# Kernel optimization log

Hardware: AMD Instinct MI355X
Metric: run time of the kernel (lower is better)

## Reference

```python
import jax, jax.numpy as jnp
import numpy as np

N, E, F, D, C, L, H = 50000, 800000, 256, 128, 40, 5, 8
HD = D // H
EPS = 1e-5


def setup_inputs() -> dict:
    key = jax.random.key(0)
    keys = iter(jax.random.split(key, 40))
    def w(shape, fan_in):
        return jax.random.normal(next(keys), shape, jnp.float32) / np.sqrt(fan_in)
    return dict(
        x=jax.random.normal(next(keys), (N, F), jnp.float32),
        edge_src=jax.random.randint(next(keys), (E,), 0, N, jnp.int32),
        edge_dst=jax.random.randint(next(keys), (E,), 0, N, jnp.int32),
        Wi=w((F, D), F), bi=jnp.zeros((D,), jnp.float32),
        Wq=w((L, D, D), D), bq=jnp.zeros((L, D), jnp.float32),
        Wk=w((L, D, D), D), bk=jnp.zeros((L, D), jnp.float32),
        Wv=w((L, D, D), D), bv=jnp.zeros((L, D), jnp.float32),
        Wo=w((L, D, D), D), bo=jnp.zeros((L, D), jnp.float32),
        g1=jnp.ones((L, D), jnp.float32), b1=jnp.zeros((L, D), jnp.float32),
        Wf1=w((L, D, 2 * D), D), bf1=jnp.zeros((L, 2 * D), jnp.float32),
        Wf2=w((L, 2 * D, D), 2 * D), bf2=jnp.zeros((L, D), jnp.float32),
        g_out=jnp.ones((D,), jnp.float32), b_out=jnp.zeros((D,), jnp.float32),
        Wout=w((D, C), D), bout=jnp.zeros((C,), jnp.float32),
    )


def _ln(x, g, b):
    mu = x.mean(-1, keepdims=True)
    var = ((x - mu) ** 2).mean(-1, keepdims=True)
    return (x - mu) / jnp.sqrt(var + EPS) * g + b


def _attn(h, src, dst, Wq, bq, Wk, bk, Wv, bv, Wo, bo):
    n = h.shape[0]
    q = (h @ Wq + bq).reshape(n, H, HD)
    k = (h @ Wk + bk).reshape(n, H, HD)
    v = (h @ Wv + bv).reshape(n, H, HD)
    # u_dot_v: per-edge dot(q[src], k[dst]) per head -> [E, H]
    scores = jnp.einsum('ehd,ehd->eh', q[src], k[dst]) / np.sqrt(HD).astype(np.float32)
    # edge_softmax over incoming edges of each destination node
    m = jax.ops.segment_max(scores, dst, num_segments=n)
    ex = jnp.exp(scores - m[dst])
    denom = jax.ops.segment_sum(ex, dst, num_segments=n)
    p = ex / denom[dst]
    # u_mul_e_sum: sum_e v[src] * p  scattered to dst
    agg = jax.ops.segment_sum(v[src] * p[:, :, None], dst, num_segments=n)
    return agg.reshape(n, D) @ Wo + bo


def reference(x, edge_src, edge_dst, Wi, bi, Wq, bq, Wk, bk, Wv, bv, Wo, bo,
              g1, b1, Wf1, bf1, Wf2, bf2, g_out, b_out, Wout, bout):
    h = jax.nn.relu(x @ Wi + bi)
    for i in range(L):
        r = _ln(h, g1[i], b1[i])
        r = _attn(r, edge_src, edge_dst, Wq[i], bq[i], Wk[i], bk[i], Wv[i], bv[i], Wo[i], bo[i])
        h = h + r
        # NOTE: original module reuses norms_1 here (norms_2 unused) - reproduced
        r = _ln(h, g1[i], b1[i])
        r = jax.nn.relu(r @ Wf1[i] + bf1[i]) @ Wf2[i] + bf2[i]
        h = h + r
    mid = h
    out = _ln(h, g_out, b_out) @ Wout + bout  # squeeze(1) is a no-op (nclass != 1)
    return (mid, out)
```

## Files before the change

kernel.cpp:

```cpp
#include <hip/hip_runtime.h>
#include <hip/hip_bf16.h>

typedef __hip_bfloat16 bf16;
typedef __attribute__((ext_vector_type(8))) short bf16x8;
typedef __attribute__((ext_vector_type(4))) float f32x4;

#define N_NODES 50000
#define N_EDGES 800000
#define DIM 128
#define QKVW 384

__device__ __forceinline__ void storeO(float* p, float v){ *p = v; }
__device__ __forceinline__ void storeO(bf16* p, float v){ *p = __float2bfloat16(v); }
__device__ __forceinline__ float bfu2f(unsigned short u){
  return __uint_as_float(((unsigned)u) << 16);
}
__device__ __forceinline__ unsigned short f2bfbits(float f){
  bf16 t = __float2bfloat16(f);
  return *reinterpret_cast<unsigned short*>(&t);
}

__global__ void fill_kernel(unsigned* __restrict__ p, unsigned val, int n){
  int i = blockIdx.x * blockDim.x + threadIdx.x;
  if (i < n) p[i] = val;
}

__global__ void prep_w_kernel(const float* __restrict__ W, bf16* __restrict__ Wt,
    int K, int M, int L){
  int idx = blockIdx.x * blockDim.x + threadIdx.x;
  int tot = L * K * M;
  if (idx >= tot) return;
  int l = idx / (K * M), r = idx - l * (K * M);
  int m = r / K, k = r - m * K;
  Wt[idx] = __float2bfloat16(W[(size_t)l * K * M + (size_t)k * M + m]);
}

__global__ void prep_qkvw_kernel(const float* __restrict__ Wq, const float* __restrict__ Wk,
    const float* __restrict__ Wv, bf16* __restrict__ Wt){
  int idx = blockIdx.x * blockDim.x + threadIdx.x;
  if (idx >= 5 * QKVW * 128) return;
  int l = idx / (QKVW * 128), r = idx - l * (QKVW * 128);
  int m = r / 128, k = r - m * 128;
  const float* src = (m < 128) ? (Wq + (size_t)l * 16384 + (size_t)k * 128 + m)
                   : (m < 256) ? (Wv + (size_t)l * 16384 + (size_t)k * 128 + (m - 128))
                               : (Wk + (size_t)l * 16384 + (size_t)k * 128 + (m - 256));
  Wt[idx] = __float2bfloat16(*src);
}

__global__ void pack_qkvbias_kernel(const float* __restrict__ bq, const float* __restrict__ bk,
    const float* __restrict__ bv, float* __restrict__ bqkv){
  int i = blockIdx.x * blockDim.x + threadIdx.x;
  if (i >= 5 * QKVW) return;
  int l = i / QKVW, j = i - l * QKVW;
  float v = (j < 128) ? bq[l * 128 + j] : (j < 256) ? bv[l * 128 + j - 128] : bk[l * 128 + j - 256];
  bqkv[i] = v;
}

__global__ void hist_kernel(const int* __restrict__ dst, int* __restrict__ counts, int E){
  int e = blockIdx.x * blockDim.x + threadIdx.x;
  if (e < E) atomicAdd(counts + dst[e], 1);
}

__global__ __launch_bounds__(256) void blockscan_kernel(const int* __restrict__ counts,
    int* __restrict__ rowptr, int* __restrict__ bsum, int n){
  __shared__ int buf[256];
  int t = threadIdx.x, i = blockIdx.x * 256 + t;
  int x = (i < n) ? counts[i] : 0;
  buf[t] = x; __syncthreads();
  #pragma unroll
  for (int off = 1; off < 256; off <<= 1){
    int v = (t >= off) ? buf[t - off] : 0;
    __syncthreads(); buf[t] += v; __syncthreads();
  }
  if (i < n) rowptr[i] = buf[t] - x;
  if (t == 255) bsum[blockIdx.x] = buf[255];
}

__global__ __launch_bounds__(256) void scanb_kernel(int* __restrict__ bsum, int nb){
  __shared__ int buf[256];
  int t = threadIdx.x;
  int x = (t < nb) ? bsum[t] : 0;
  buf[t] = x; __syncthreads();
  #pragma unroll
  for (int off = 1; off < 256; off <<= 1){
    int v = (t >= off) ? buf[t - off] : 0;
    __syncthreads(); buf[t] += v; __syncthreads();
  }
  if (t < nb) bsum[t] = buf[t] - x;
  if (t == nb - 1) bsum[nb] = buf[t];
}

__global__ void addoff_kernel(int* __restrict__ rowptr, const int* __restrict__ bsum,
    int n, int nb){
  int i = blockIdx.x * blockDim.x + threadIdx.x;
  if (i < n) rowptr[i] += bsum[i >> 8];
  if (i == 0) rowptr[n] = bsum[nb];
}

__global__ void scatter_kernel(const int* __restrict__ src, const int* __restrict__ dst,
    const int* __restrict__ rowptr, int* __restrict__ cursor,
    int* __restrict__ srclist, int E){
  int e = blockIdx.x * blockDim.x + threadIdx.x;
  if (e >= E) return;
  int d = dst[e];
  int pos = rowptr[d] + atomicAdd(cursor + d, 1);
  srclist[pos] = src[e];
}

__global__ __launch_bounds__(256) void attn_kernel(
    const int* __restrict__ rowptr, const int* __restrict__ srclist,
    const bf16* __restrict__ qkv, bf16* __restrict__ agg, int n){
  int d = blockIdx.x * 4 + (threadIdx.x >> 6);
  int lane = threadIdx.x & 63;
  if (d >= n) return;
  int eslot = lane >> 4;
  int t = lane & 15;
  float kf[8];
  {
    const int4* kp = (const int4*)(qkv + (size_t)d * QKVW + 256 + t * 8);
    int4 kv = kp[0];
    const unsigned* ku = (const unsigned*)&kv;
    #pragma unroll
    for (int j = 0; j < 4; j++){
      kf[2*j]   = __uint_as_float(ku[j] << 16) * 0.25f;
      kf[2*j+1] = __uint_as_float(ku[j] & 0xffff0000u) * 0.25f;
    }
  }
  float acc[8];
  #pragma unroll
  for (int j = 0; j < 8; j++) acc[j] = 0.f;
  float den = 0.f;
  int e = rowptr[d], e1 = rowptr[d + 1];
  for (; e < e1; e += 8){
    int eeA = e + eslot, eeB = e + 4 + eslot;
    int sA = srclist[(eeA < e1) ? eeA : (e1 - 1)];
    int sB = srclist[(eeB < e1) ? eeB : (e1 - 1)];
    const int4* qpA = (const int4*)(qkv + (size_t)sA * QKVW + t * 8);
    const int4* qpB = (const int4*)(qkv + (size_t)sB * QKVW + t * 8);
    int4 qA = qpA[0];
    int4 vA = qpA[16];
    int4 qB = qpB[0];
    int4 vB = qpB[16];
    float pA = 0.f, pB = 0.f;
    const unsigned* qa = (const unsigned*)&qA;
    const unsigned* qb = (const unsigned*)&qB;
    #pragma unroll
    for (int j = 0; j < 4; j++){
      pA = fmaf(__uint_as_float(qa[j] << 16),          kf[2*j],   pA);
      pA = fmaf(__uint_as_float(qa[j] & 0xffff0000u),  kf[2*j+1], pA);
      pB = fmaf(__uint_as_float(qb[j] << 16),          kf[2*j],   pB);
      pB = fmaf(__uint_as_float(qb[j] & 0xffff0000u),  kf[2*j+1], pB);
    }
    pA += __shfl_xor(pA, 1);
    pB += __shfl_xor(pB, 1);
    float wA = (eeA < e1) ? __expf(pA) : 0.f;
    float wB = (eeB < e1) ? __expf(pB) : 0.f;
    den += wA + wB;
    const unsigned* va = (const unsigned*)&vA;
    const unsigned* vb = (const unsigned*)&vB;
    #pragma unroll
    for (int j = 0; j < 4; j++){
      acc[2*j]   = fmaf(wA, __uint_as_float(va[j] << 16),         acc[2*j]);
      acc[2*j+1] = fmaf(wA, __uint_as_float(va[j] & 0xffff0000u), acc[2*j+1]);
      acc[2*j]   = fmaf(wB, __uint_as_float(vb[j] << 16),         acc[2*j]);
      acc[2*j+1] = fmaf(wB, __uint_as_float(vb[j] & 0xffff0000u), acc[2*j+1]);
    }
  }
  #pragma unroll
  for (int m = 16; m <= 32; m <<= 1){
    den += __shfl_xor(den, m);
    #pragma unroll
    for (int j = 0; j < 8; j++) acc[j] += __shfl_xor(acc[j], m);
  }
  if (eslot == 0){
    float inv = (den > 0.f) ? 1.f / den : 0.f;
    unsigned short o[8];
    #pragma unroll
    for (int j = 0; j < 8; j++) o[j] = f2bfbits(acc[j] * inv);
    *(int4*)(agg + (size_t)d * DIM + t * 8) = *(const int4*)o;
  }
}

template<int KT, int MT, typename AT, bool FUSELN, bool RELU, bool RESID, typename OT>
__global__ __launch_bounds__(256, (KT == 128) ? 4 : 2) void pgemm4(
    const AT* __restrict__ A, const float* __restrict__ lng, const float* __restrict__ lnb,
    const bf16* __restrict__ Wt, const float* __restrict__ bias,
    const float* __restrict__ resid, OT* __restrict__ out, float* __restrict__ out2,
    int n, int M){
  constexpr int CPR = KT / 8;
  constexpr int CPT = (64 * CPR) / 256;
  constexpr int NMT = MT / 64;
  constexpr int NKS = KT / 32;
  __shared__ short Ash[64][KT + 8];
  int tid = threadIdx.x;
  int wv = tid >> 6, lane = tid & 63;
  int l15 = lane & 15, quad = lane >> 4;
  int bm = blockIdx.x * 64;

  bf16x8 wf[2][NKS];
  auto loadW = [&](int mt, int b){
    int col = mt * 64 + wv * 16 + l15;
    #pragma unroll
    for (int ks = 0; ks < NKS; ks++){
      int4 w = make_int4(0, 0, 0, 0);
      if (col < M) w = *(const int4*)(Wt + (size_t)col * KT + ks * 32 + quad * 8);
      wf[b][ks] = *(bf16x8*)&w;
    }
  };
  loadW(0, 0);

  #pragma unroll
  for (int i = 0; i < CPT; i++){
    int c = tid + i * 256;
    int row = c / CPR, off = (c - row * CPR) * 8;
    int gr = bm + row;
    if constexpr (sizeof(AT) == 4){
      float va[8];
      if (gr < n){
        float4 f0 = *(const float4*)(A + (size_t)gr * KT + off);
        float4 f1 = *(const float4*)(A + (size_t)gr * KT + off + 4);
        va[0]=f0.x; va[1]=f0.y; va[2]=f0.z; va[3]=f0.w;
        va[4]=f1.x; va[5]=f1.y; va[6]=f1.z; va[7]=f1.w;
      } else {
        #pragma unroll
        for (int j = 0; j < 8; j++) va[j] = 0.f;
      }
      if constexpr (FUSELN){
        float s = va[0]+va[1]+va[2]+va[3]+va[4]+va[5]+va[6]+va[7];
        s += __shfl_xor(s, 1); s += __shfl_xor(s, 2);
        s += __shfl_xor(s, 4); s += __shfl_xor(s, 8);
        float mu = s * (1.f / 128.f);
        float vs = 0.f;
        #pragma unroll
        for (int j = 0; j < 8; j++){ float dd = va[j] - mu; vs += dd * dd; }
        vs += __shfl_xor(vs, 1); vs += __shfl_xor(vs, 2);
        vs += __shfl_xor(vs, 4); vs += __shfl_xor(vs, 8);
        float rs = rsqrtf(vs * (1.f / 128.f) + 1e-5f);
        float4 g0 = *(const float4*)(lng + off);
        float4 g1 = *(const float4*)(lng + off + 4);
        float4 b0 = *(const float4*)(lnb + off);
        float4 b1 = *(const float4*)(lnb + off + 4);
        va[0]=(va[0]-mu)*rs*g0.x+b0.x; va[1]=(va[1]-mu)*rs*g0.y+b0.y;
        va[2]=(va[2]-mu)*rs*g0.z+b0.z; va[3]=(va[3]-mu)*rs*g0.w+b0.w;
        va[4]=(va[4]-mu)*rs*g1.x+b1.x; va[5]=(va[5]-mu)*rs*g1.y+b1.y;
        va[6]=(va[6]-mu)*rs*g1.z+b1.z; va[7]=(va[7]-mu)*rs*g1.w+b1.w;
      }
      unsigned short tmp[8];
      #pragma unroll
      for (int j = 0; j < 8; j++) tmp[j] = f2bfbits(va[j]);
      *(int4*)(&Ash[row][off]) = *(const int4*)tmp;
    } else {
      int4 av = make_int4(0, 0, 0, 0);
      if (gr < n) av = *(const int4*)(A + (size_t)gr * KT + off);
      *(int4*)(&Ash[row][off]) = av;
    }
  }
  __syncthreads();

  #pragma unroll
  for (int mt = 0; mt < NMT; mt++){
    int b = mt & 1;
    if (mt + 1 < NMT) loadW(mt + 1, b ^ 1);
    f32x4 acc[4];
    #pragma unroll
    for (int i = 0; i < 4; i++) acc[i] = (f32x4){0.f, 0.f, 0.f, 0.f};
    #pragma unroll
    for (int ks = 0; ks < NKS; ks++){
      bf16x8 bfrag = wf[b][ks];
      #pragma unroll
      for (int mi = 0; mi < 4; mi++){
        bf16x8 afrag = *(const bf16x8*)(&Ash[mi * 16 + l15][ks * 32 + quad * 8]);
        acc[mi] = __builtin_amdgcn_mfma_f32_16x16x32_bf16(afrag, bfrag, acc[mi], 0, 0, 0);
      }
    }
    int col = mt * 64 + wv * 16 + l15;
    if (col < M){
      float bval = bias[col];
      #pragma unroll
      for (int mi = 0; mi < 4; mi++){
        int row0 = bm + mi * 16 + quad * 4;
        #pragma unroll
        for (int rg = 0; rg < 4; rg++){
          int grow = row0 + rg;
          if (grow >= n) continue;
          float v = acc[mi][rg] + bval;
          if (RELU) v = fmaxf(v, 0.f);
          if (RESID) v += resid[(size_t)grow * M + col];
          storeO(out + (size_t)grow * M + col, v);
          if (out2) out2[(size_t)grow * M + col] = v;
        }
      }
    }
  }
}

extern "C" void kernel_launch(void* const* d_in, const int* in_sizes, int n_in,
                              void* d_out, int out_size, void* d_ws, size_t ws_size,
                              hipStream_t stream) {
  const float* x    = (const float*)d_in[0];
  const int*  esrc  = (const int*)d_in[1];
  const int*  edst  = (const int*)d_in[2];
  const float* Wi   = (const float*)d_in[3];
  const float* bi   = (const float*)d_in[4];
  const float* Wq   = (const float*)d_in[5];
  const float* bq   = (const float*)d_in[6];
  const float* Wk   = (const float*)d_in[7];
  const float* bk   = (const float*)d_in[8];
  const float* Wv   = (const float*)d_in[9];
  const float* bv   = (const float*)d_in[10];
  const float* Wo   = (const float*)d_in[11];
  const float* bo   = (const float*)d_in[12];
  const float* g1   = (const float*)d_in[13];
  const float* b1   = (const float*)d_in[14];
  const float* Wf1  = (const float*)d_in[15];
  const float* bf1  = (const float*)d_in[16];
  const float* Wf2  = (const float*)d_in[17];
  const float* bf2  = (const float*)d_in[18];
  const float* gout = (const float*)d_in[19];
  const float* bout_ln = (const float*)d_in[20];
  const float* Wout = (const float*)d_in[21];
  const float* bout = (const float*)d_in[22];

  const size_t ND = (size_t)N_NODES * DIM;
  float* ws = (float*)d_ws;
  float* h   = ws;
  bf16* agg  = (bf16*)(ws + ND);
  bf16* qkv  = (bf16*)(ws + ND + ND / 2);
  bf16* mid  = qkv;
  float* after_qkv = ws + ND + ND / 2 + ((size_t)N_NODES * QKVW) / 2;
  bf16* Wit    = (bf16*)after_qkv;
  bf16* Wqkvt  = Wit + 128 * 256;
  bf16* Wot    = Wqkvt + 5 * QKVW * 128;
  bf16* Wf1t   = Wot + 5 * 128 * 128;
  bf16* Wf2t   = Wf1t + 5 * 256 * 128;
  bf16* Woutt  = Wf2t + 5 * 128 * 256;
  float* bqkv  = (float*)(Woutt + 40 * 128);
  int* rowptr  = (int*)(bqkv + 5 * QKVW);
  int* cnt     = rowptr + N_NODES + 1;
  int* bsum    = cnt + N_NODES;
  int* srclist = bsum + 200;

  dim3 B(256);
  const int EB = (N_EDGES + 255) / 256;
  const int NB = (N_NODES + 255) / 256;
  const int NSB = (N_NODES + 255) / 256;
  dim3 Grow(782);

  prep_w_kernel<<<(1 * 256 * 128 + 255) / 256, B, 0, stream>>>(Wi, Wit, 256, 128, 1);
  prep_qkvw_kernel<<<(5 * QKVW * 128 + 255) / 256, B, 0, stream>>>(Wq, Wk, Wv, Wqkvt);
  prep_w_kernel<<<(5 * 128 * 128 + 255) / 256, B, 0, stream>>>(Wo, Wot, 128, 128, 5);
  prep_w_kernel<<<(5 * 128 * 256 + 255) / 256, B, 0, stream>>>(Wf1, Wf1t, 128, 256, 5);
  prep_w_kernel<<<(5 * 256 * 128 + 255) / 256, B, 0, stream>>>(Wf2, Wf2t, 256, 128, 5);
  prep_w_kernel<<<(1 * 128 * 40 + 255) / 256, B, 0, stream>>>(Wout, Woutt, 128, 40, 1);
  pack_qkvbias_kernel<<<(5 * QKVW + 255) / 256, B, 0, stream>>>(bq, bk, bv, bqkv);
  fill_kernel<<<NB, B, 0, stream>>>((unsigned*)cnt, 0u, N_NODES);
  hist_kernel<<<EB, B, 0, stream>>>(edst, cnt, N_EDGES);
  blockscan_kernel<<<NSB, B, 0, stream>>>(cnt, rowptr, bsum, N_NODES);
  scanb_kernel<<<1, B, 0, stream>>>(bsum, NSB);
  addoff_kernel<<<NB, B, 0, stream>>>(rowptr, bsum, N_NODES, NSB);
  fill_kernel<<<NB, B, 0, stream>>>((unsigned*)cnt, 0u, N_NODES);
  scatter_kernel<<<EB, B, 0, stream>>>(esrc, edst, rowptr, cnt, srclist, N_EDGES);

  pgemm4<256, 128, float, false, true, false, float><<<Grow, B, 0, stream>>>(
      x, nullptr, nullptr, Wit, bi, nullptr, h, nullptr, N_NODES, 128);

  for (int l = 0; l < 5; l++){
    pgemm4<128, 384, float, true, false, false, bf16><<<Grow, B, 0, stream>>>(
        h, g1 + l * DIM, b1 + l * DIM, Wqkvt + (size_t)l * QKVW * 128,
        bqkv + l * QKVW, nullptr, qkv, nullptr, N_NODES, QKVW);
    attn_kernel<<<12500, B, 0, stream>>>(rowptr, srclist, qkv, agg, N_NODES);
    pgemm4<128, 128, bf16, false, false, true, float><<<Grow, B, 0, stream>>>(
        agg, nullptr, nullptr, Wot + (size_t)l * 128 * 128, bo + l * DIM,
        h, h, nullptr, N_NODES, 128);
    pgemm4<128, 256, float, true, true, false, bf16><<<Grow, B, 0, stream>>>(
        h, g1 + l * DIM, b1 + l * DIM, Wf1t + (size_t)l * 256 * 128,
        bf1 + l * 2 * DIM, nullptr, mid, nullptr, N_NODES, 256);
    float* out2 = (l == 4) ? (float*)d_out : nullptr;
    pgemm4<256, 128, bf16, false, false, true, float><<<Grow, B, 0, stream>>>(
        mid, nullptr, nullptr, Wf2t + (size_t)l * 128 * 256, bf2 + l * DIM,
        h, h, out2, N_NODES, 128);
  }

  pgemm4<128, 64, float, true, false, false, float><<<Grow, B, 0, stream>>>(
      h, gout, bout_ln, Woutt, bout, nullptr, ((float*)d_out) + ND, nullptr, N_NODES, 40);
}
```

Baseline: 1.060 ms.

## Fuse consecutive GEMMs through shared-memory LayerNorm into a two-stage kernel

Replaces the single-GEMM kernel with a fused kernel that computes a 128-wide GEMM with bias, residual and ReLU, writes h, then LayerNorms the tile in shared memory and runs the following GEMM (QKV, FFN1 or output head). This chains input-proj→QKV, Wo→FFN1 and FFN2→next QKV or head, so h is never re-read from global memory for the LN-fused GEMMs, and the launch count drops. It uses more shared memory and registers per block and computes variance as E[x²]−mu², which is less numerically stable. The mid buffer is moved to its own region so it no longer aliases qkv.

```diff
diff --git a/kernel.cpp b/kernel.cpp
--- a/kernel.cpp
+++ b/kernel.cpp
@@ -181,113 +181,183 @@
   }
 }
 
-template<int KT, int MT, typename AT, bool FUSELN, bool RELU, bool RESID, typename OT>
-__global__ __launch_bounds__(256, (KT == 128) ? 4 : 2) void pgemm4(
-    const AT* __restrict__ A, const float* __restrict__ lng, const float* __restrict__ lnb,
-    const bf16* __restrict__ Wt, const float* __restrict__ bias,
-    const float* __restrict__ resid, OT* __restrict__ out, float* __restrict__ out2,
-    int n, int M){
-  constexpr int CPR = KT / 8;
+template<int KT1, typename AT1, bool RELU1, bool RESID, int M2T, bool RELU2, typename OT2>
+__global__ __launch_bounds__(256, (KT1 == 128) ? 4 : 3) void fgemm(
+    const AT1* __restrict__ A, const bf16* __restrict__ W1t, const float* __restrict__ b1v,
+    const float* __restrict__ resid, float* __restrict__ hout, float* __restrict__ outd,
+    const float* __restrict__ lng, const float* __restrict__ lnb,
+    const bf16* __restrict__ W2t, const float* __restrict__ b2v,
+    OT2* __restrict__ out2nd, int n, int M2rt){
+  constexpr int NKS1 = KT1 / 32;
+  constexpr int NMT2 = M2T / 64;
+  constexpr int CPR = KT1 / 8;
   constexpr int CPT = (64 * CPR) / 256;
-  constexpr int NMT = MT / 64;
-  constexpr int NKS = KT / 32;
-  __shared__ short Ash[64][KT + 8];
+  __shared__ short Ash[64][KT1 + 8];
+  __shared__ short Ash2[64][136];
+  __shared__ float2 sred[4][64];
   int tid = threadIdx.x;
   int wv = tid >> 6, lane = tid & 63;
   int l15 = lane & 15, quad = lane >> 4;
   int bm = blockIdx.x * 64;
 
-  bf16x8 wf[2][NKS];
-  auto loadW = [&](int mt, int b){
+  bf16x8 wf[NKS1];
+  auto loadW1 = [&](int mt){
     int col = mt * 64 + wv * 16 + l15;
     #pragma unroll
-    for (int ks = 0; ks < NKS; ks++){
-      int4 w = make_int4(0, 0, 0, 0);
-      if (col < M) w = *(const int4*)(Wt + (size_t)col * KT + ks * 32 + quad * 8);
-      wf[b][ks] = *(bf16x8*)&w;
+    for (int ks = 0; ks < NKS1; ks++){
+      int4 w = *(const int4*)(W1t + (size_t)col * KT1 + ks * 32 + quad * 8);
+      wf[ks] = *(bf16x8*)&w;
     }
   };
-  loadW(0, 0);
+  loadW1(0);
 
   #pragma unroll
   for (int i = 0; i < CPT; i++){
     int c = tid + i * 256;
     int row = c / CPR, off = (c - row * CPR) * 8;
     int gr = bm + row;
-    if constexpr (sizeof(AT) == 4){
+    if constexpr (sizeof(AT1) == 4){
       float va[8];
       if (gr < n){
-        float4 f0 = *(const float4*)(A + (size_t)gr * KT + off);
-        float4 f1 = *(const float4*)(A + (size_t)gr * KT + off + 4);
+        float4 f0 = *(const float4*)(A + (size_t)gr * KT1 + off);
+        float4 f1 = *(const float4*)(A + (size_t)gr * KT1 + off + 4);
         va[0]=f0.x; va[1]=f0.y; va[2]=f0.z; va[3]=f0.w;
         va[4]=f1.x; va[5]=f1.y; va[6]=f1.z; va[7]=f1.w;
       } else {
         #pragma unroll
         for (int j = 0; j < 8; j++) va[j] = 0.f;
       }
-      if constexpr (FUSELN){
-        float s = va[0]+va[1]+va[2]+va[3]+va[4]+va[5]+va[6]+va[7];
-        s += __shfl_xor(s, 1); s += __shfl_xor(s, 2);
-        s += __shfl_xor(s, 4); s += __shfl_xor(s, 8);
-        float mu = s * (1.f / 128.f);
-        float vs = 0.f;
-        #pragma unroll
-        for (int j = 0; j < 8; j++){ float dd = va[j] - mu; vs += dd * dd; }
-        vs += __shfl_xor(vs, 1); vs += __shfl_xor(vs, 2);
-        vs += __shfl_xor(vs, 4); vs += __shfl_xor(vs, 8);
-        float rs = rsqrtf(vs * (1.f / 128.f) + 1e-5f);
-        float4 g0 = *(const float4*)(lng + off);
-        float4 g1 = *(const float4*)(lng + off + 4);
-        float4 b0 = *(const float4*)(lnb + off);
-        float4 b1 = *(const float4*)(lnb + off + 4);
-        va[0]=(va[0]-mu)*rs*g0.x+b0.x; va[1]=(va[1]-mu)*rs*g0.y+b0.y;
-        va[2]=(va[2]-mu)*rs*g0.z+b0.z; va[3]=(va[3]-mu)*rs*g0.w+b0.w;
-        va[4]=(va[4]-mu)*rs*g1.x+b1.x; va[5]=(va[5]-mu)*rs*g1.y+b1.y;
-        va[6]=(va[6]-mu)*rs*g1.z+b1.z; va[7]=(va[7]-mu)*rs*g1.w+b1.w;
-      }
       unsigned short tmp[8];
       #pragma unroll
       for (int j = 0; j < 8; j++) tmp[j] = f2bfbits(va[j]);
       *(int4*)(&Ash[row][off]) = *(const int4*)tmp;
     } else {
       int4 av = make_int4(0, 0, 0, 0);
-      if (gr < n) av = *(const int4*)(A + (size_t)gr * KT + off);
+      if (gr < n) av = *(const int4*)(A + (size_t)gr * KT1 + off);
       *(int4*)(&Ash[row][off]) = av;
     }
   }
   __syncthreads();
 
-  #pragma unroll
-  for (int mt = 0; mt < NMT; mt++){
-    int b = mt & 1;
-    if (mt + 1 < NMT) loadW(mt + 1, b ^ 1);
-    f32x4 acc[4];
-    #pragma unroll
-    for (int i = 0; i < 4; i++) acc[i] = (f32x4){0.f, 0.f, 0.f, 0.f};
-    #pragma unroll
-    for (int ks = 0; ks < NKS; ks++){
-      bf16x8 bfrag = wf[b][ks];
+  f32x4 acc[2][4];
+  #pragma unroll
+  for (int mt = 0; mt < 2; mt++)
+    #pragma unroll
+    for (int mi = 0; mi < 4; mi++) acc[mt][mi] = (f32x4){0.f, 0.f, 0.f, 0.f};
+  #pragma unroll
+  for (int mt = 0; mt < 2; mt++){
+    if (mt) loadW1(1);
+    #pragma unroll
+    for (int ks = 0; ks < NKS1; ks++){
+      bf16x8 bfrag = wf[ks];
       #pragma unroll
       for (int mi = 0; mi < 4; mi++){
         bf16x8 afrag = *(const bf16x8*)(&Ash[mi * 16 + l15][ks * 32 + quad * 8]);
-        acc[mi] = __builtin_amdgcn_mfma_f32_16x16x32_bf16(afrag, bfrag, acc[mi], 0, 0, 0);
-      }
-    }
+        acc[mt][mi] = __builtin_amdgcn_mfma_f32_16x16x32_bf16(afrag, bfrag, acc[mt][mi], 0, 0, 0);
+      }
+    }
+  }
+
+  int colv[2] = { wv * 16 + l15, 64 + wv * 16 + l15 };
+  float b1c[2] = { b1v[colv[0]], b1v[colv[1]] };
+  #pragma unroll
+  for (int mt = 0; mt < 2; mt++){
+    #pragma unroll
+    for (int mi = 0; mi < 4; mi++){
+      #pragma unroll
+      for (int rg = 0; rg < 4; rg++){
+        int grow = bm + mi * 16 + quad * 4 + rg;
+        float v = acc[mt][mi][rg] + b1c[mt];
+        if (RESID && grow < n) v += resid[(size_t)grow * 128 + colv[mt]];
+        if (RELU1) v = fmaxf(v, 0.f);
+        acc[mt][mi][rg] = v;
+        if (grow < n){
+          hout[(size_t)grow * 128 + colv[mt]] = v;
+          if (outd) outd[(size_t)grow * 128 + colv[mt]] = v;
+        }
+      }
+    }
+  }
+  #pragma unroll
+  for (int mi = 0; mi < 4; mi++){
+    #pragma unroll
+    for (int rg = 0; rg < 4; rg++){
+      float s = acc[0][mi][rg] + acc[1][mi][rg];
+      float q = acc[0][mi][rg] * acc[0][mi][rg] + acc[1][mi][rg] * acc[1][mi][rg];
+      s += __shfl_xor(s, 1); q += __shfl_xor(q, 1);
+      s += __shfl_xor(s, 2); q += __shfl_xor(q, 2);
+      s += __shfl_xor(s, 4); q += __shfl_xor(q, 4);
+      s += __shfl_xor(s, 8); q += __shfl_xor(q, 8);
+      if (l15 == 0) sred[wv][mi * 16 + quad * 4 + rg] = make_float2(s, q);
+    }
+  }
+  __syncthreads();
+  if (tid < 64){
+    float2 a0 = sred[0][tid], a1 = sred[1][tid], a2 = sred[2][tid], a3 = sred[3][tid];
+    float s = a0.x + a1.x + a2.x + a3.x;
+    float q = a0.y + a1.y + a2.y + a3.y;
+    float mu = s * (1.f / 128.f);
+    float var = q * (1.f / 128.f) - mu * mu;
+    float rs = rsqrtf(fmaxf(var, 0.f) + 1e-5f);
+    sred[0][tid] = make_float2(mu, rs);
+  }
+  __syncthreads();
+  float gg[2] = { lng[colv[0]], lng[colv[1]] };
+  float bb[2] = { lnb[colv[0]], lnb[colv[1]] };
+  #pragma unroll
+  for (int mi = 0; mi < 4; mi++){
+    #pragma unroll
+    for (int rg = 0; rg < 4; rg++){
+      int row = mi * 16 + quad * 4 + rg;
+      float2 ms = sred[0][row];
+      #pragma unroll
+      for (int mt = 0; mt < 2; mt++){
+        float hv = (acc[mt][mi][rg] - ms.x) * ms.y * gg[mt] + bb[mt];
+        Ash2[row][colv[mt]] = (short)f2bfbits(hv);
+      }
+    }
+  }
+  __syncthreads();
+
+  bf16x8 wf2[2][4];
+  auto loadW2 = [&](int mt, int b){
     int col = mt * 64 + wv * 16 + l15;
-    if (col < M){
-      float bval = bias[col];
+    #pragma unroll
+    for (int ks = 0; ks < 4; ks++){
+      int4 w = make_int4(0, 0, 0, 0);
+      if (col < M2rt) w = *(const int4*)(W2t + (size_t)col * 128 + ks * 32 + quad * 8);
+      wf2[b][ks] = *(bf16x8*)&w;
+    }
+  };
+  loadW2(0, 0);
+  #pragma unroll
+  for (int mt = 0; mt < NMT2; mt++){
+    int b = mt & 1;
+    if (mt + 1 < NMT2) loadW2(mt + 1, b ^ 1);
+    f32x4 a2[4];
+    #pragma unroll
+    for (int i = 0; i < 4; i++) a2[i] = (f32x4){0.f, 0.f, 0.f, 0.f};
+    #pragma unroll
+    for (int ks = 0; ks < 4; ks++){
+      bf16x8 bfrag = wf2[b][ks];
       #pragma unroll
       for (int mi = 0; mi < 4; mi++){
-        int row0 = bm + mi * 16 + quad * 4;
+        bf16x8 afrag = *(const bf16x8*)(&Ash2[mi * 16 + l15][ks * 32 + quad * 8]);
+        a2[mi] = __builtin_amdgcn_mfma_f32_16x16x32_bf16(afrag, bfrag, a2[mi], 0, 0, 0);
+      }
+    }
+    int col = mt * 64 + wv * 16 + l15;
+    if (col < M2rt){
+      float bval = b2v[col];
+      #pragma unroll
+      for (int mi = 0; mi < 4; mi++){
         #pragma unroll
         for (int rg = 0; rg < 4; rg++){
-          int grow = row0 + rg;
+          int grow = bm + mi * 16 + quad * 4 + rg;
           if (grow >= n) continue;
-          float v = acc[mi][rg] + bval;
-          if (RELU) v = fmaxf(v, 0.f);
-          if (RESID) v += resid[(size_t)grow * M + col];
-          storeO(out + (size_t)grow * M + col, v);
-          if (out2) out2[(size_t)grow * M + col] = v;
+          float v = a2[mi][rg] + bval;
+          if (RELU2) v = fmaxf(v, 0.f);
+          storeO(out2nd + (size_t)grow * M2rt + col, v);
         }
       }
     }
@@ -326,9 +396,9 @@
   float* h   = ws;
   bf16* agg  = (bf16*)(ws + ND);
   bf16* qkv  = (bf16*)(ws + ND + ND / 2);
-  bf16* mid  = qkv;
-  float* after_qkv = ws + ND + ND / 2 + ((size_t)N_NODES * QKVW) / 2;
-  bf16* Wit    = (bf16*)after_qkv;
+  bf16* mid  = qkv + (size_t)N_NODES * QKVW;
+  float* after_mid = ws + ND + ND / 2 + ((size_t)N_NODES * (QKVW + 256)) / 2;
+  bf16* Wit    = (bf16*)after_mid;
   bf16* Wqkvt  = Wit + 128 * 256;
   bf16* Wot    = Wqkvt + 5 * QKVW * 128;
   bf16* Wf1t   = Wot + 5 * 128 * 128;
@@ -361,26 +431,27 @@
   fill_kernel<<<NB, B, 0, stream>>>((unsigned*)cnt, 0u, N_NODES);
   scatter_kernel<<<EB, B, 0, stream>>>(esrc, edst, rowptr, cnt, srclist, N_EDGES);
 
-  pgemm4<256, 128, float, false, true, false, float><<<Grow, B, 0, stream>>>(
-      x, nullptr, nullptr, Wit, bi, nullptr, h, nullptr, N_NODES, 128);
+  fgemm<256, float, true, false, 384, false, bf16><<<Grow, B, 0, stream>>>(
+      x, Wit, bi, nullptr, h, nullptr, g1, b1,
+      Wqkvt, bqkv, qkv, N_NODES, QKVW);
 
   for (int l = 0; l < 5; l++){
-    pgemm4<128, 384, float, true, false, false, bf16><<<Grow, B, 0, stream>>>(
-        h, g1 + l * DIM, b1 + l * DIM, Wqkvt + (size_t)l * QKVW * 128,
-        bqkv + l * QKVW, nullptr, qkv, nullptr, N_NODES, QKVW);
     attn_kernel<<<12500, B, 0, stream>>>(rowptr, srclist, qkv, agg, N_NODES);
-    pgemm4<128, 128, bf16, false, false, true, float><<<Grow, B, 0, stream>>>(
-        agg, nullptr, nullptr, Wot + (size_t)l * 128 * 128, bo + l * DIM,
-        h, h, nullptr, N_NODES, 128);
-    pgemm4<128, 256, float, true, true, false, bf16><<<Grow, B, 0, stream>>>(
-        h, g1 + l * DIM, b1 + l * DIM, Wf1t + (size_t)l * 256 * 128,
-        bf1 + l * 2 * DIM, nullptr, mid, nullptr, N_NODES, 256);
-    float* out2 = (l == 4) ? (float*)d_out : nullptr;
-    pgemm4<256, 128, bf16, false, false, true, float><<<Grow, B, 0, stream>>>(
-        mid, nullptr, nullptr, Wf2t + (size_t)l * 128 * 256, bf2 + l * DIM,
-        h, h, out2, N_NODES, 128);
-  }
-
-  pgemm4<128, 64, float, true, false, false, float><<<Grow, B, 0, stream>>>(
-      h, gout, bout_ln, Woutt, bout, nullptr, ((float*)d_out) + ND, nullptr, N_NODES, 40);
-}
+    fgemm<128, bf16, false, true, 256, true, bf16><<<Grow, B, 0, stream>>>(
+        agg, Wot + (size_t)l * 128 * 128, bo + l * DIM, h, h, nullptr,
+        g1 + l * DIM, b1 + l * DIM,
+        Wf1t + (size_t)l * 256 * 128, bf1 + l * 2 * DIM, mid, N_NODES, 256);
+    if (l < 4){
+      fgemm<256, bf16, false, true, 384, false, bf16><<<Grow, B, 0, stream>>>(
+          mid, Wf2t + (size_t)l * 128 * 256, bf2 + l * DIM, h, h, nullptr,
+          g1 + (l + 1) * DIM, b1 + (l + 1) * DIM,
+          Wqkvt + (size_t)(l + 1) * QKVW * 128, bqkv + (l + 1) * QKVW,
+          qkv, N_NODES, QKVW);
+    } else {
+      fgemm<256, bf16, false, true, 64, false, float><<<Grow, B, 0, stream>>>(
+          mid, Wf2t + (size_t)l * 128 * 256, bf2 + l * DIM, h, h, (float*)d_out,
+          gout, bout_ln,
+          Woutt, bout, ((float*)d_out) + ND, N_NODES, 40);
+    }
+  }
+}
```

Measured after the change: 1.248 ms. 17.7% more time.
